# Performance work log

Measured on AMD Instinct MI355X. Metric: run time of the kernel, lower is better.

## Reference

```python
import jax, jax.numpy as jnp
import numpy as np

TOP_K = 8
SCORE_FUNC = "sigmoid"
ROUTE_NORM = True
ROUTE_SCALE = 2.5


def setup_inputs() -> dict:
    key = jax.random.key(0)
    k1, k2, k3 = jax.random.split(key, 3)
    B, S, H, E = 4, 4096, 2048, 64
    hidden_states = jax.random.normal(k1, (B, S, H), dtype=jnp.float32)
    # nn.Linear default init scale ~ 1/sqrt(H); exact distribution irrelevant for correctness
    gate_w = jax.random.normal(k2, (E, H), dtype=jnp.float32) * (1.0 / np.sqrt(H))
    expert_bias = jax.random.normal(k3, (E,), dtype=jnp.float32) * 0.1
    return {"hidden_states": hidden_states, "expert_bias": expert_bias, "gate_w": gate_w}


def reference(hidden_states, expert_bias, gate_w):
    B, S, H = hidden_states.shape
    x = hidden_states.reshape(-1, H)  # [T, H]
    logits = jnp.einsum("th,eh->te", x, gate_w)  # [T, E]
    if SCORE_FUNC == "sigmoid":
        scores = jax.nn.sigmoid(logits.astype(jnp.float32))
    else:
        scores = jax.nn.softmax(logits.astype(jnp.float32), axis=-1)
    if expert_bias is not None:
        _, selected_experts = jax.lax.top_k(scores + expert_bias[None, :], TOP_K)
        top_scores = jnp.take_along_axis(scores, selected_experts, axis=1)
    else:
        top_scores, selected_experts = jax.lax.top_k(scores, TOP_K)
    if SCORE_FUNC == "sigmoid" and ROUTE_NORM:
        denom = jnp.sum(top_scores, axis=-1, keepdims=True) + 1e-20
        top_scores = top_scores / denom
    top_scores = top_scores * ROUTE_SCALE
    return top_scores, selected_experts
```

## Files before the change

### kernel.cpp

```cpp
#include <hip/hip_runtime.h>
#include <math.h>

#define T_TOTAL 16384
#define HDIM    2048
#define NEXP    64

template<int KS>
__global__ __launch_bounds__(256, 4)
void router_gemm_kernel(const float* __restrict__ x,
                        const float* __restrict__ w,
                        float* __restrict__ partial)
{
    constexpr int KSLICE = HDIM / KS;
    constexpr int BK    = 16;
    constexpr int XS_ST = 258;
    constexpr int WS_ST = 66;

    __shared__ float Xs[BK][XS_ST];
    __shared__ float Ws[BK][WS_ST];

    const int tid = threadIdx.x;
    const int tb  = blockIdx.x & 63;
    const int ks  = blockIdx.x >> 6;
    const int t0  = tb * 256;
    const int k0  = ks * KSLICE;

    const int kq  = tid & 3;
    const int rr  = tid >> 2;

    const int eg8 = (tid & 7) * 8;
    const int tg8 = (tid >> 3) * 8;

    float acc[8][8];
#pragma unroll
    for (int i = 0; i < 8; ++i)
#pragma unroll
        for (int j = 0; j < 8; ++j) acc[i][j] = 0.0f;

#pragma unroll 1
    for (int kc = 0; kc < KSLICE; kc += BK) {
        __syncthreads();

        {
            const float* xg = x + (size_t)t0 * HDIM + (k0 + kc) + kq * 4;
#pragma unroll
            for (int p = 0; p < 4; ++p) {
                const int r = p * 64 + rr;
                const float4 v = *(const float4*)(xg + (size_t)r * HDIM);
                Xs[kq * 4 + 0][r] = v.x;
                Xs[kq * 4 + 1][r] = v.y;
                Xs[kq * 4 + 2][r] = v.z;
                Xs[kq * 4 + 3][r] = v.w;
            }
        }
        {
            const float4 v = *(const float4*)(w + (size_t)rr * HDIM + (k0 + kc) + kq * 4);
            Ws[kq * 4 + 0][rr] = v.x;
            Ws[kq * 4 + 1][rr] = v.y;
            Ws[kq * 4 + 2][rr] = v.z;
            Ws[kq * 4 + 3][rr] = v.w;
        }
        __syncthreads();

#pragma unroll
        for (int k = 0; k < BK; ++k) {
            float xv[8], wv[8];
#pragma unroll
            for (int i = 0; i < 8; ++i) xv[i] = Xs[k][tg8 + i];
#pragma unroll
            for (int j = 0; j < 8; ++j) wv[j] = Ws[k][eg8 + j];
#pragma unroll
            for (int i = 0; i < 8; ++i)
#pragma unroll
                for (int j = 0; j < 8; ++j)
                    acc[i][j] = fmaf(xv[i], wv[j], acc[i][j]);
        }
    }

    float* pp = partial + ((size_t)(t0 + tg8) * KS + ks) * NEXP + eg8;
#pragma unroll
    for (int i = 0; i < 8; ++i) {
        float* q = pp + (size_t)i * KS * NEXP;
        *(float4*)(q)     = make_float4(acc[i][0], acc[i][1], acc[i][2], acc[i][3]);
        *(float4*)(q + 4) = make_float4(acc[i][4], acc[i][5], acc[i][6], acc[i][7]);
    }
}

__global__ __launch_bounds__(256)
void router_topk_kernel(const float* __restrict__ partial,
                        const float* __restrict__ bias,
                        float* __restrict__ out_scores,
                        float* __restrict__ out_idx,
                        int ksCount)
{
    const int token = blockIdx.x * 4 + (threadIdx.x >> 6);
    const int lane  = threadIdx.x & 63;

    const float* pt = partial + (size_t)token * ksCount * NEXP + lane;
    float logit = 0.0f;
    for (int s = 0; s < ksCount; ++s) logit += pt[(size_t)s * NEXP];

    const float score = 1.0f / (1.0f + expf(-logit));
    float key = score + bias[lane];

    float myscore = 0.0f;
    int   myidx   = 0;
    float denom   = 0.0f;

#pragma unroll
    for (int r = 0; r < 8; ++r) {
        float bk = key;
        int   bi = lane;
#pragma unroll
        for (int off = 32; off > 0; off >>= 1) {
            const float ok = __shfl_xor(bk, off);
            const int   oi = __shfl_xor(bi, off);
            if (ok > bk || (ok == bk && oi < bi)) { bk = ok; bi = oi; }
        }
        const float wsc = __shfl(score, bi);
        denom += wsc;
        if (lane == r)  { myscore = wsc; myidx = bi; }
        if (lane == bi) key = -__builtin_inff();
    }

    const float factor = 2.5f / (denom + 1e-20f);
    if (lane < 8) {
        out_scores[(size_t)token * 8 + lane] = myscore * factor;
        out_idx  [(size_t)token * 8 + lane] = (float)myidx;
    }
}

extern "C" void kernel_launch(void* const* d_in, const int* in_sizes, int n_in,
                              void* d_out, int out_size, void* d_ws, size_t ws_size,
                              hipStream_t stream)
{
    const float* x    = (const float*)d_in[0];
    const float* bias = (const float*)d_in[1];
    const float* w    = (const float*)d_in[2];

    float* out     = (float*)d_out;
    float* partial = (float*)d_ws;

    const size_t bytesPerSlice = (size_t)T_TOTAL * NEXP * 4;

    int ksCount;
    if (ws_size >= 16 * bytesPerSlice) {
        ksCount = 16;
        router_gemm_kernel<16><<<dim3(64 * 16), dim3(256), 0, stream>>>(x, w, partial);
    } else {
        ksCount = 4;
        router_gemm_kernel<4><<<dim3(64 * 4), dim3(256), 0, stream>>>(x, w, partial);
    }

    router_topk_kernel<<<dim3(T_TOTAL / 4), dim3(256), 0, stream>>>(
        partial, bias, out, out + (size_t)T_TOTAL * 8, ksCount);
}
```

Before: 251.8 us.

## Read gate weights via wave-uniform scalar loads and re-tile per-lane tokens

The gate weights are no longer staged in shared memory. Each wave owns 16 experts and reads their weights directly from global memory with wave-uniform addresses, which can become scalar loads. Each lane now computes 4 tokens × 16 experts, reading X from shared memory as float4 vectors, which cuts shared-memory read traffic per FMA. A KS=8 split is added as an intermediate fallback for smaller workspaces. The risk is scalar-load latency stalling the FMA stream if those loads are not prefetched well.

```diff
diff --git a/kernel.cpp b/kernel.cpp
--- a/kernel.cpp
+++ b/kernel.cpp
@@ -12,30 +12,31 @@
                         float* __restrict__ partial)
 {
     constexpr int KSLICE = HDIM / KS;
-    constexpr int BK    = 16;
-    constexpr int XS_ST = 258;
-    constexpr int WS_ST = 66;
+    constexpr int BK     = 16;
+    constexpr int XS_ST  = 260;
 
-    __shared__ float Xs[BK][XS_ST];
-    __shared__ float Ws[BK][WS_ST];
+    __shared__ __align__(16) float Xs[BK][XS_ST];
 
-    const int tid = threadIdx.x;
-    const int tb  = blockIdx.x & 63;
-    const int ks  = blockIdx.x >> 6;
-    const int t0  = tb * 256;
-    const int k0  = ks * KSLICE;
+    const int tid  = threadIdx.x;
+    const int lane = tid & 63;
+    const int wv   = __builtin_amdgcn_readfirstlane(tid >> 6);
+    const int tb   = blockIdx.x & 63;
+    const int ks   = blockIdx.x >> 6;
+    const int t0   = tb * 256;
+    const int k0   = ks * KSLICE;
 
-    const int kq  = tid & 3;
-    const int rr  = tid >> 2;
+    const int e0   = wv * 16;
+    const int kq   = tid & 3;
+    const int rr   = tid >> 2;
+    const int l4   = lane * 4;
 
-    const int eg8 = (tid & 7) * 8;
-    const int tg8 = (tid >> 3) * 8;
+    const float* wb = w + (size_t)e0 * HDIM + k0;
 
-    float acc[8][8];
+    float acc[4][16];
 #pragma unroll
-    for (int i = 0; i < 8; ++i)
+    for (int t = 0; t < 4; ++t)
 #pragma unroll
-        for (int j = 0; j < 8; ++j) acc[i][j] = 0.0f;
+        for (int j = 0; j < 16; ++j) acc[t][j] = 0.0f;
 
 #pragma unroll 1
     for (int kc = 0; kc < KSLICE; kc += BK) {
@@ -53,36 +54,47 @@
                 Xs[kq * 4 + 3][r] = v.w;
             }
         }
-        {
-            const float4 v = *(const float4*)(w + (size_t)rr * HDIM + (k0 + kc) + kq * 4);
-            Ws[kq * 4 + 0][rr] = v.x;
-            Ws[kq * 4 + 1][rr] = v.y;
-            Ws[kq * 4 + 2][rr] = v.z;
-            Ws[kq * 4 + 3][rr] = v.w;
-        }
         __syncthreads();
 
 #pragma unroll
-        for (int k = 0; k < BK; ++k) {
-            float xv[8], wv[8];
+        for (int kk = 0; kk < BK; kk += 4) {
+            float4 xr[4];
 #pragma unroll
-            for (int i = 0; i < 8; ++i) xv[i] = Xs[k][tg8 + i];
+            for (int c = 0; c < 4; ++c)
+                xr[c] = *(const float4*)&Xs[kk + c][l4];
+
 #pragma unroll
-            for (int j = 0; j < 8; ++j) wv[j] = Ws[k][eg8 + j];
-#pragma unroll
-            for (int i = 0; i < 8; ++i)
-#pragma unroll
-                for (int j = 0; j < 8; ++j)
-                    acc[i][j] = fmaf(xv[i], wv[j], acc[i][j]);
+            for (int j = 0; j < 16; ++j) {
+                const float* wr = wb + (size_t)j * HDIM + (kc + kk);
+                const float w0 = wr[0], w1 = wr[1], w2 = wr[2], w3 = wr[3];
+                acc[0][j] = fmaf(xr[0].x, w0, acc[0][j]);
+                acc[1][j] = fmaf(xr[0].y, w0, acc[1][j]);
+                acc[2][j] = fmaf(xr[0].z, w0, acc[2][j]);
+                acc[3][j] = fmaf(xr[0].w, w0, acc[3][j]);
+                acc[0][j] = fmaf(xr[1].x, w1, acc[0][j]);
+                acc[1][j] = fmaf(xr[1].y, w1, acc[1][j]);
+                acc[2][j] = fmaf(xr[1].z, w1, acc[2][j]);
+                acc[3][j] = fmaf(xr[1].w, w1, acc[3][j]);
+                acc[0][j] = fmaf(xr[2].x, w2, acc[0][j]);
+                acc[1][j] = fmaf(xr[2].y, w2, acc[1][j]);
+                acc[2][j] = fmaf(xr[2].z, w2, acc[2][j]);
+                acc[3][j] = fmaf(xr[2].w, w2, acc[3][j]);
+                acc[0][j] = fmaf(xr[3].x, w3, acc[0][j]);
+                acc[1][j] = fmaf(xr[3].y, w3, acc[1][j]);
+                acc[2][j] = fmaf(xr[3].z, w3, acc[2][j]);
+                acc[3][j] = fmaf(xr[3].w, w3, acc[3][j]);
+            }
         }
     }
 
-    float* pp = partial + ((size_t)(t0 + tg8) * KS + ks) * NEXP + eg8;
+    float* pp = partial + ((size_t)(t0 + l4) * KS + ks) * NEXP + e0;
 #pragma unroll
-    for (int i = 0; i < 8; ++i) {
-        float* q = pp + (size_t)i * KS * NEXP;
-        *(float4*)(q)     = make_float4(acc[i][0], acc[i][1], acc[i][2], acc[i][3]);
-        *(float4*)(q + 4) = make_float4(acc[i][4], acc[i][5], acc[i][6], acc[i][7]);
+    for (int t = 0; t < 4; ++t) {
+        float* q = pp + (size_t)t * KS * NEXP;
+        *(float4*)(q +  0) = make_float4(acc[t][ 0], acc[t][ 1], acc[t][ 2], acc[t][ 3]);
+        *(float4*)(q +  4) = make_float4(acc[t][ 4], acc[t][ 5], acc[t][ 6], acc[t][ 7]);
+        *(float4*)(q +  8) = make_float4(acc[t][ 8], acc[t][ 9], acc[t][10], acc[t][11]);
+        *(float4*)(q + 12) = make_float4(acc[t][12], acc[t][13], acc[t][14], acc[t][15]);
     }
 }
 
@@ -147,6 +159,9 @@
     if (ws_size >= 16 * bytesPerSlice) {
         ksCount = 16;
         router_gemm_kernel<16><<<dim3(64 * 16), dim3(256), 0, stream>>>(x, w, partial);
+    } else if (ws_size >= 8 * bytesPerSlice) {
+        ksCount = 8;
+        router_gemm_kernel<8><<<dim3(64 * 8), dim3(256), 0, stream>>>(x, w, partial);
     } else {
         ksCount = 4;
         router_gemm_kernel<4><<<dim3(64 * 4), dim3(256), 0, stream>>>(x, w, partial);
```

Result: slower. 337.9 us (+34.2%).
